# Kernel tuning notes

Hardware: AMD Instinct MI355X
Metric: run time of the kernel (lower is better)

The kernel has to match this reference:

```python
import jax, jax.numpy as jnp
import numpy as np

D_MODEL = 1024
NUM_HEADS = 16
D_K = D_MODEL // NUM_HEADS
BATCH = 2
SEQ = 2048


def setup_inputs() -> dict:
    key = jax.random.key(0)
    ks = jax.random.split(key, 11)
    s = 1.0 / np.sqrt(D_MODEL)
    return {
        "query": jax.random.normal(ks[0], (BATCH, SEQ, D_MODEL), jnp.float32),
        "key_": jax.random.normal(ks[1], (BATCH, SEQ, D_MODEL), jnp.float32),
        "value": jax.random.normal(ks[2], (BATCH, SEQ, D_MODEL), jnp.float32),
        "w_q": jax.random.uniform(ks[3], (D_MODEL, D_MODEL), jnp.float32, -s, s),
        "b_q": jax.random.uniform(ks[4], (D_MODEL,), jnp.float32, -s, s),
        "w_k": jax.random.uniform(ks[5], (D_MODEL, D_MODEL), jnp.float32, -s, s),
        "b_k": jax.random.uniform(ks[6], (D_MODEL,), jnp.float32, -s, s),
        "w_v": jax.random.uniform(ks[7], (D_MODEL, D_MODEL), jnp.float32, -s, s),
        "b_v": jax.random.uniform(ks[8], (D_MODEL,), jnp.float32, -s, s),
        "w_o": jax.random.uniform(ks[9], (D_MODEL, D_MODEL), jnp.float32, -s, s),
        "b_o": jax.random.uniform(ks[10], (D_MODEL,), jnp.float32, -s, s),
    }


def reference(query, key_, value, w_q, b_q, w_k, b_k, w_v, b_v, w_o, b_o):
    B, S, D = query.shape
    H, dk = NUM_HEADS, D_K

    def proj(x, w, b):
        # torch Linear: x @ w.T + b ; reshape to (B, H, S, dk)
        return (x @ w.T + b).reshape(B, S, H, dk).transpose(0, 2, 1, 3)

    Q = proj(query, w_q, b_q)
    K = proj(key_, w_k, b_k)
    V = proj(value, w_v, b_v)

    scores = jnp.einsum("bhqd,bhkd->bhqk", Q, K) / jnp.sqrt(jnp.float32(dk))
    attn = jax.nn.softmax(scores, axis=-1)  # dropout is identity in eval
    ctx = jnp.einsum("bhqk,bhkd->bhqd", attn, V)
    ctx = ctx.transpose(0, 2, 1, 3).reshape(B, S, D)
    out = ctx @ w_o.T + b_o
    return out
```

## Files before the change

kernel.cpp:

```cpp
#include <hip/hip_runtime.h>
#include <cstdint>
#include <cstddef>

typedef unsigned short u16;
typedef short bf16x8 __attribute__((ext_vector_type(8)));
typedef unsigned short u16x8 __attribute__((ext_vector_type(8)));
typedef float f32x4 __attribute__((ext_vector_type(4)));

#define NHEAD 16
#define SEQ 2048
#define DMODEL 1024
#define BATCH 2
#define QSCALE 0.18033688011112042f

__device__ __forceinline__ float exp2_fast(float x) {
  return __builtin_amdgcn_exp2f(x);
}

__device__ __forceinline__ u16 f2bf(float f) {
  union { float f; unsigned u; } v; v.f = f;
  return (u16)((v.u + 0x7fffu + ((v.u >> 16) & 1u)) >> 16);
}

__device__ __forceinline__ unsigned cvt_pk(float a, float b) {
  unsigned r;
  asm("v_cvt_pk_bf16_f32 %0, %1, %2" : "=v"(r) : "v"(a), "v"(b));
  return r;
}

__device__ __forceinline__ int swz(int row, int colbyte) {
  return (row << 7) + (colbyte ^ ((row & 7) << 4));
}

__device__ __forceinline__ void load_lds16(const void* g, void* lds) {
  __builtin_amdgcn_global_load_lds(
      (const __attribute__((address_space(1))) unsigned int*)g,
      (__attribute__((address_space(3))) unsigned int*)lds, 16, 0, 0);
}

__global__ __launch_bounds__(256) void wconv(
    const float* __restrict__ wq, const float* __restrict__ wk,
    const float* __restrict__ wv, const float* __restrict__ wo,
    u16* __restrict__ Wq, u16* __restrict__ Wk, u16* __restrict__ Wv,
    u16* __restrict__ Wo) {
  int bid = blockIdx.x;
  int a = bid >> 9;
  int local = bid & 511;
  const float* in = a == 0 ? wq : a == 1 ? wk : a == 2 ? wv : wo;
  u16* out = a == 0 ? Wq : a == 1 ? Wk : a == 2 ? Wv : Wo;
  int i = local * 256 + threadIdx.x;
  const float4* p = (const float4*)in + (size_t)i * 2;
  float4 a4 = p[0], b4 = p[1];
  u16x8 o;
  o[0] = f2bf(a4.x); o[1] = f2bf(a4.y); o[2] = f2bf(a4.z); o[3] = f2bf(a4.w);
  o[4] = f2bf(b4.x); o[5] = f2bf(b4.y); o[6] = f2bf(b4.z); o[7] = f2bf(b4.w);
  *((u16x8*)out + i) = o;
}

__global__ __launch_bounds__(256) void gemm_qkv(
    const float* __restrict__ A0, const float* __restrict__ A1, const float* __restrict__ A2,
    const u16* __restrict__ W0, const u16* __restrict__ W1, const u16* __restrict__ W2,
    const float* __restrict__ b0, const float* __restrict__ b1, const float* __restrict__ b2,
    u16* __restrict__ C0, u16* __restrict__ C1, u16* __restrict__ C2) {
  constexpr int K = 1024;
  __shared__ u16 Ash[128 * 32];
  __shared__ u16 Bsh[128 * 32];
  const int z = blockIdx.z;
  const float* A = z == 0 ? A0 : z == 1 ? A1 : A2;
  const u16* W = z == 0 ? W0 : z == 1 ? W1 : W2;
  const float* bias = z == 0 ? b0 : z == 1 ? b1 : b2;
  u16* C = z == 0 ? C0 : z == 1 ? C1 : C2;
  const float scale = z == 0 ? QSCALE : 1.0f;

  const int t = threadIdx.x;
  const int w = t >> 6;
  const int l = t & 63;
  const int m0 = (blockIdx.x * 4 + (blockIdx.y >> 3)) * 128;
  const int n0 = (blockIdx.y & 7) * 128;
  const int wm = (w >> 1) * 64;
  const int wn = (w & 1) * 64;
  const int lr = l & 15;
  const int hi = l >> 4;
  const int lk = hi * 8;
  const int srow = l >> 2;
  const int scol = (l & 3) * 8;
  const int ssw = ((l >> 3) & 3) << 3;
  const int ar = t >> 2;
  const int ac = (t & 3) * 8;
  const int asw = ((ar >> 1) & 3) << 3;
  const int fsw = ((lr >> 1) & 3) << 3;

  f32x4 acc[4][4] = {};

  const float* Abase0 = A + (size_t)(m0 + ar) * K;
  const float* Abase1 = A + (size_t)(m0 + 64 + ar) * K;
  f32x4 f0 = *(const f32x4*)&Abase0[ac];
  f32x4 f1 = *(const f32x4*)&Abase0[ac + 4];
  f32x4 f2 = *(const f32x4*)&Abase1[ac];
  f32x4 f3 = *(const f32x4*)&Abase1[ac + 4];

  for (int k0 = 0; k0 < K; k0 += 32) {
#pragma unroll
    for (int c = 0; c < 2; ++c) {
      int rb = (c * 4 + w) * 16 + srow;
      load_lds16(W + (size_t)(n0 + rb) * K + k0 + (scol ^ ssw), &Bsh[(c * 4 + w) * 512]);
    }
    {
      uint4 o;
      o.x = cvt_pk(f0[0], f0[1]); o.y = cvt_pk(f0[2], f0[3]);
      o.z = cvt_pk(f1[0], f1[1]); o.w = cvt_pk(f1[2], f1[3]);
      *(uint4*)&Ash[ar * 32 + (ac ^ asw)] = o;
      o.x = cvt_pk(f2[0], f2[1]); o.y = cvt_pk(f2[2], f2[3]);
      o.z = cvt_pk(f3[0], f3[1]); o.w = cvt_pk(f3[2], f3[3]);
      *(uint4*)&Ash[(64 + ar) * 32 + (ac ^ asw)] = o;
    }
    if (k0 + 32 < K) {
      f0 = *(const f32x4*)&Abase0[k0 + 32 + ac];
      f1 = *(const f32x4*)&Abase0[k0 + 32 + ac + 4];
      f2 = *(const f32x4*)&Abase1[k0 + 32 + ac];
      f3 = *(const f32x4*)&Abase1[k0 + 32 + ac + 4];
    }
    __syncthreads();
    bf16x8 af[4], bfr[4];
#pragma unroll
    for (int i = 0; i < 4; ++i)
      af[i] = *(const bf16x8*)&Ash[(wm + i * 16 + lr) * 32 + (lk ^ fsw)];
#pragma unroll
    for (int j = 0; j < 4; ++j)
      bfr[j] = *(const bf16x8*)&Bsh[(wn + j * 16 + lr) * 32 + (lk ^ fsw)];
#pragma unroll
    for (int i = 0; i < 4; ++i)
#pragma unroll
      for (int j = 0; j < 4; ++j)
        acc[i][j] = __builtin_amdgcn_mfma_f32_16x16x32_bf16(af[i], bfr[j], acc[i][j], 0, 0, 0);
    __syncthreads();
  }

#pragma unroll
  for (int i = 0; i < 4; ++i)
#pragma unroll
    for (int j = 0; j < 4; ++j)
#pragma unroll
      for (int r = 0; r < 4; ++r) {
        int row = m0 + wm + i * 16 + hi * 4 + r;
        int col = n0 + wn + j * 16 + lr;
        float v = (acc[i][j][r] + bias[col]) * scale;
        int b = row >> 11, s = row & 2047;
        int h = col >> 6, d = col & 63;
        C[(((size_t)(b * NHEAD + h) * SEQ + s) << 6) + d] = f2bf(v);
      }
}

__global__ __launch_bounds__(256) void gemm_o(const u16* __restrict__ A,
                                              const u16* __restrict__ W,
                                              const float* __restrict__ bias,
                                              float* __restrict__ C) {
  constexpr int K = 1024;
  __shared__ u16 Ash[64 * 32];
  __shared__ u16 Bsh[128 * 32];
  const int t = threadIdx.x;
  const int w = t >> 6;
  const int l = t & 63;
  const int m0 = (blockIdx.x * 8 + (blockIdx.y >> 3)) * 64;
  const int n0 = (blockIdx.y & 7) * 128;
  const int wm = (w >> 1) * 32;
  const int wn = (w & 1) * 64;
  const int lr = l & 15;
  const int hi = l >> 4;
  const int lk = hi * 8;
  const int srow = l >> 2;
  const int scol = (l & 3) * 8;
  const int ssw = ((l >> 3) & 3) << 3;
  const int fsw = ((lr >> 1) & 3) << 3;

  f32x4 acc[2][4] = {};

  for (int k0 = 0; k0 < K; k0 += 32) {
    {
      int ra = w * 16 + srow;
      load_lds16(A + (size_t)(m0 + ra) * K + k0 + (scol ^ ssw), &Ash[w * 512]);
    }
#pragma unroll
    for (int c = 0; c < 2; ++c) {
      int rb = (c * 4 + w) * 16 + srow;
      load_lds16(W + (size_t)(n0 + rb) * K + k0 + (scol ^ ssw), &Bsh[(c * 4 + w) * 512]);
    }
    __syncthreads();
    bf16x8 af[2], bfr[4];
#pragma unroll
    for (int i = 0; i < 2; ++i)
      af[i] = *(const bf16x8*)&Ash[(wm + i * 16 + lr) * 32 + (lk ^ fsw)];
#pragma unroll
    for (int j = 0; j < 4; ++j)
      bfr[j] = *(const bf16x8*)&Bsh[(wn + j * 16 + lr) * 32 + (lk ^ fsw)];
#pragma unroll
    for (int i = 0; i < 2; ++i)
#pragma unroll
      for (int j = 0; j < 4; ++j)
        acc[i][j] = __builtin_amdgcn_mfma_f32_16x16x32_bf16(af[i], bfr[j], acc[i][j], 0, 0, 0);
    __syncthreads();
  }

#pragma unroll
  for (int i = 0; i < 2; ++i)
#pragma unroll
    for (int j = 0; j < 4; ++j)
#pragma unroll
      for (int r = 0; r < 4; ++r) {
        int row = m0 + wm + i * 16 + hi * 4 + r;
        int col = n0 + wn + j * 16 + lr;
        C[(size_t)row * DMODEL + col] = acc[i][j][r] + bias[col];
      }
}

__global__ __launch_bounds__(256) void transpose_v(const u16* __restrict__ V,
                                                   u16* __restrict__ Vt) {
  __shared__ u16 tile[64][72];
  int st = blockIdx.x, bh = blockIdx.y;
  int t = threadIdx.x;
  {
    int s = t >> 2, part = (t & 3) * 16;
    const u16* g = V + (((size_t)bh * SEQ + st * 64 + s) << 6) + part;
    u16x8 v0 = *(const u16x8*)&g[0];
    u16x8 v1 = *(const u16x8*)&g[8];
    *(u16x8*)&tile[s][part] = v0;
    *(u16x8*)&tile[s][part + 8] = v1;
  }
  __syncthreads();
  {
    int d = t >> 2, sp = (t & 3) * 16;
    u16x8 o0, o1;
#pragma unroll
    for (int j = 0; j < 8; ++j) {
      int c0 = sp + j, c1 = sp + 8 + j;
      o0[j] = tile[(c0 & 3) * 16 + (c0 >> 2)][d];
      o1[j] = tile[(c1 & 3) * 16 + (c1 >> 2)][d];
    }
    u16* out = Vt + ((size_t)bh * 64 + d) * SEQ + st * 64 + sp;
    *(u16x8*)&out[0] = o0;
    *(u16x8*)&out[8] = o1;
  }
}

__device__ __forceinline__ void attn_tile(
    int kt, bool pf, const u16* Kg, const u16* Vg, int srow, int scb,
    char* QsB, char* KsC, char* VsC, char* KsN, char* VsN,
    bf16x8 (&qf)[2][2], f32x4 (&acc)[2][4], float (&lsum)[2][4],
    int w, int lr, int hi) {
  u16x8 nk0, nk1, nv0, nv1;
  if (pf) {
    const u16* kg = Kg + (kt + 1) * 4096;
    const u16* vg = Vg + (kt + 1) * 64;
    nk0 = *(const u16x8*)&kg[srow * 64 + scb / 2];
    nk1 = *(const u16x8*)&kg[srow * 64 + scb / 2 + 8];
    nv0 = *(const u16x8*)&vg[(size_t)srow * SEQ + scb / 2];
    nv1 = *(const u16x8*)&vg[(size_t)srow * SEQ + scb / 2 + 8];
  }

  f32x4 sc[2][4] = {};
  __builtin_amdgcn_s_setprio(1);
#pragma unroll
  for (int ks = 0; ks < 2; ++ks) {
    bf16x8 kb[4];
#pragma unroll
    for (int nt = 0; nt < 4; ++nt)
      kb[nt] = *(const bf16x8*)(KsC + swz(nt * 16 + lr, ks * 64 + hi * 16));
#pragma unroll
    for (int mt = 0; mt < 2; ++mt)
#pragma unroll
      for (int nt = 0; nt < 4; ++nt)
        sc[mt][nt] = __builtin_amdgcn_mfma_f32_16x16x32_bf16(qf[mt][ks], kb[nt], sc[mt][nt], 0, 0, 0);
  }
  __builtin_amdgcn_s_setprio(0);

#pragma unroll
  for (int mt = 0; mt < 2; ++mt)
#pragma unroll
    for (int r = 0; r < 4; ++r) {
      int prow = w * 32 + mt * 16 + hi * 4 + r;
      float p0 = exp2_fast(sc[mt][0][r]);
      float p1 = exp2_fast(sc[mt][1][r]);
      float p2 = exp2_fast(sc[mt][2][r]);
      float p3 = exp2_fast(sc[mt][3][r]);
      lsum[mt][r] += (p0 + p1) + (p2 + p3);
      uint2 pk;
      pk.x = cvt_pk(p0, p1);
      pk.y = cvt_pk(p2, p3);
      *(uint2*)(QsB + swz(prow, lr * 8)) = pk;
    }

  asm volatile("" ::: "memory");

  __builtin_amdgcn_s_setprio(1);
#pragma unroll
  for (int ks = 0; ks < 2; ++ks) {
    bf16x8 pa[2], vb[4];
#pragma unroll
    for (int mt = 0; mt < 2; ++mt)
      pa[mt] = *(const bf16x8*)(QsB + swz(w * 32 + mt * 16 + lr, ks * 64 + hi * 16));
#pragma unroll
    for (int nt = 0; nt < 4; ++nt)
      vb[nt] = *(const bf16x8*)(VsC + swz(nt * 16 + lr, ks * 64 + hi * 16));
#pragma unroll
    for (int mt = 0; mt < 2; ++mt)
#pragma unroll
      for (int nt = 0; nt < 4; ++nt)
        acc[mt][nt] = __builtin_amdgcn_mfma_f32_16x16x32_bf16(pa[mt], vb[nt], acc[mt][nt], 0, 0, 0);
  }
  __builtin_amdgcn_s_setprio(0);

  if (pf) {
    *(u16x8*)(KsN + swz(srow, scb)) = nk0;
    *(u16x8*)(KsN + swz(srow, scb + 16)) = nk1;
    *(u16x8*)(VsN + swz(srow, scb)) = nv0;
    *(u16x8*)(VsN + swz(srow, scb + 16)) = nv1;
  }
  __syncthreads();
}

__global__ __launch_bounds__(256) void attn(const u16* __restrict__ Q,
                                            const u16* __restrict__ K,
                                            const u16* __restrict__ Vt,
                                            u16* __restrict__ ctx) {
  __shared__ u16 Qs[128 * 64];
  __shared__ u16 Ks[2][64 * 64];
  __shared__ u16 Vs[2][64 * 64];
  char* const QsB = (char*)Qs;

  const int t = threadIdx.x, w = t >> 6, l = t & 63;
  const int lr = l & 15, hi = l >> 4;

  const int bid = blockIdx.x;
  const int idx = bid >> 3;
  const int bh = (bid & 7) * 4 + (idx >> 4);
  const int q0 = (idx & 15) * 128;

  const u16* Qg = Q + ((size_t)bh * SEQ + q0) * 64;
  const u16* Kg = K + (size_t)bh * SEQ * 64;
  const u16* Vg = Vt + (size_t)bh * 64 * SEQ;

#pragma unroll
  for (int i = 0; i < 4; ++i) {
    int c = i * 256 + t;
    int row = c >> 3, cb = (c & 7) * 16;
    u16x8 qv = *(const u16x8*)&Qg[row * 64 + cb / 2];
    *(u16x8*)(QsB + swz(row, cb)) = qv;
  }
  const int srow = t >> 2;
  const int scb = (t & 3) * 32;
  {
    u16x8 k0 = *(const u16x8*)&Kg[srow * 64 + scb / 2];
    u16x8 k1 = *(const u16x8*)&Kg[srow * 64 + scb / 2 + 8];
    u16x8 v0 = *(const u16x8*)&Vg[(size_t)srow * SEQ + scb / 2];
    u16x8 v1 = *(const u16x8*)&Vg[(size_t)srow * SEQ + scb / 2 + 8];
    char* KsB = (char*)Ks[0];
    char* VsB = (char*)Vs[0];
    *(u16x8*)(KsB + swz(srow, scb)) = k0;
    *(u16x8*)(KsB + swz(srow, scb + 16)) = k1;
    *(u16x8*)(VsB + swz(srow, scb)) = v0;
    *(u16x8*)(VsB + swz(srow, scb + 16)) = v1;
  }
  __syncthreads();

  bf16x8 qf[2][2];
#pragma unroll
  for (int mt = 0; mt < 2; ++mt)
#pragma unroll
    for (int ks = 0; ks < 2; ++ks)
      qf[mt][ks] = *(const bf16x8*)(QsB + swz(w * 32 + mt * 16 + lr, ks * 64 + hi * 16));

  f32x4 acc[2][4] = {};
  float lsum[2][4] = {{0.f, 0.f, 0.f, 0.f}, {0.f, 0.f, 0.f, 0.f}};

  for (int kt2 = 0; kt2 < SEQ / 128; ++kt2) {
    attn_tile(2 * kt2, true, Kg, Vg, srow, scb, QsB,
              (char*)Ks[0], (char*)Vs[0], (char*)Ks[1], (char*)Vs[1],
              qf, acc, lsum, w, lr, hi);
    attn_tile(2 * kt2 + 1, kt2 < SEQ / 128 - 1, Kg, Vg, srow, scb, QsB,
              (char*)Ks[1], (char*)Vs[1], (char*)Ks[0], (char*)Vs[0],
              qf, acc, lsum, w, lr, hi);
  }

  const int b = bh >> 4, h = bh & 15;
#pragma unroll
  for (int mt = 0; mt < 2; ++mt)
#pragma unroll
    for (int r = 0; r < 4; ++r) {
      float s = lsum[mt][r];
      s += __shfl_xor(s, 1);
      s += __shfl_xor(s, 2);
      s += __shfl_xor(s, 4);
      s += __shfl_xor(s, 8);
      float inv = 1.0f / s;
      int srow_ = q0 + w * 32 + mt * 16 + hi * 4 + r;
#pragma unroll
      for (int nt = 0; nt < 4; ++nt) {
        int d = nt * 16 + lr;
        ctx[((size_t)(b * SEQ + srow_)) * DMODEL + h * 64 + d] =
            f2bf(acc[mt][nt][r] * inv);
      }
    }
}

extern "C" void kernel_launch(void* const* d_in, const int* in_sizes, int n_in,
                              void* d_out, int out_size, void* d_ws, size_t ws_size,
                              hipStream_t stream) {
  const float* q  = (const float*)d_in[0];
  const float* k  = (const float*)d_in[1];
  const float* v  = (const float*)d_in[2];
  const float* wq = (const float*)d_in[3];
  const float* bq = (const float*)d_in[4];
  const float* wk = (const float*)d_in[5];
  const float* bk = (const float*)d_in[6];
  const float* wv = (const float*)d_in[7];
  const float* bv = (const float*)d_in[8];
  const float* wo = (const float*)d_in[9];
  const float* bo = (const float*)d_in[10];

  const size_t XB = (size_t)4096 * 1024 * 2;
  const size_t WB = (size_t)1024 * 1024 * 2;
  char* ws = (char*)d_ws;
  u16* ctxb = (u16*)(ws);
  u16* Vtb = (u16*)(ws + XB);
  u16* Wq = (u16*)(ws + 3 * XB);
  u16* Wk = (u16*)(ws + 3 * XB + WB);
  u16* Wv = (u16*)(ws + 3 * XB + 2 * WB);
  u16* Wo = (u16*)(ws + 3 * XB + 3 * WB);
  u16* Qb = (u16*)(ws + 4 * XB);
  u16* Kb = (u16*)(ws + 5 * XB);
  u16* Vb = (u16*)(ws + 6 * XB);

  wconv<<<2048, 256, 0, stream>>>(wq, wk, wv, wo, Wq, Wk, Wv, Wo);

  gemm_qkv<<<dim3(8, 32, 3), 256, 0, stream>>>(q, k, v, Wq, Wk, Wv,
                                               bq, bk, bv, Qb, Kb, Vb);

  transpose_v<<<dim3(SEQ / 64, BATCH * NHEAD), 256, 0, stream>>>(Vb, Vtb);

  attn<<<512, 256, 0, stream>>>(Qb, Kb, Vtb, ctxb);

  gemm_o<<<dim3(8, 64), 256, 0, stream>>>(ctxb, Wo, bo, (float*)d_out);
}
```

Measured before the change: 117.5 us.

## Split attention over two KV halves and merge partials in a combine kernel

Each attention block now processes only half of the key/value sequence, so the grid grows from 512 to 1024 blocks. Each block writes an unnormalised partial context in bf16 plus its per-row exp-sum. A new combine kernel adds the two partials and divides by the total sum before the output projection. This is meant to raise parallelism and occupancy in the attention stage, at the cost of an extra kernel launch, extra global traffic for the partial buffers, and an extra bf16 rounding of the unnormalised partials.

```diff
diff --git a/kernel.cpp b/kernel.cpp
--- a/kernel.cpp
+++ b/kernel.cpp
@@ -20,6 +20,10 @@
 __device__ __forceinline__ u16 f2bf(float f) {
   union { float f; unsigned u; } v; v.f = f;
   return (u16)((v.u + 0x7fffu + ((v.u >> 16) & 1u)) >> 16);
+}
+
+__device__ __forceinline__ float bf2f(u16 x) {
+  union { unsigned u; float f; } v; v.u = ((unsigned)x) << 16; return v.f;
 }
 
 __device__ __forceinline__ unsigned cvt_pk(float a, float b) {
@@ -321,7 +325,9 @@
 __global__ __launch_bounds__(256) void attn(const u16* __restrict__ Q,
                                             const u16* __restrict__ K,
                                             const u16* __restrict__ Vt,
-                                            u16* __restrict__ ctx) {
+                                            u16* __restrict__ N1,
+                                            u16* __restrict__ N2,
+                                            float* __restrict__ Lb) {
   __shared__ u16 Qs[128 * 64];
   __shared__ u16 Ks[2][64 * 64];
   __shared__ u16 Vs[2][64 * 64];
@@ -332,8 +338,11 @@
 
   const int bid = blockIdx.x;
   const int idx = bid >> 3;
-  const int bh = (bid & 7) * 4 + (idx >> 4);
-  const int q0 = (idx & 15) * 128;
+  const int bh = (bid & 7) * 4 + (idx >> 5);
+  const int rem = idx & 31;
+  const int q0 = (rem >> 1) * 128;
+  const int half = rem & 1;
+  const int base = half * 16;
 
   const u16* Qg = Q + ((size_t)bh * SEQ + q0) * 64;
   const u16* Kg = K + (size_t)bh * SEQ * 64;
@@ -349,10 +358,12 @@
   const int srow = t >> 2;
   const int scb = (t & 3) * 32;
   {
-    u16x8 k0 = *(const u16x8*)&Kg[srow * 64 + scb / 2];
-    u16x8 k1 = *(const u16x8*)&Kg[srow * 64 + scb / 2 + 8];
-    u16x8 v0 = *(const u16x8*)&Vg[(size_t)srow * SEQ + scb / 2];
-    u16x8 v1 = *(const u16x8*)&Vg[(size_t)srow * SEQ + scb / 2 + 8];
+    const u16* kg = Kg + base * 4096;
+    const u16* vg = Vg + base * 64;
+    u16x8 k0 = *(const u16x8*)&kg[srow * 64 + scb / 2];
+    u16x8 k1 = *(const u16x8*)&kg[srow * 64 + scb / 2 + 8];
+    u16x8 v0 = *(const u16x8*)&vg[(size_t)srow * SEQ + scb / 2];
+    u16x8 v1 = *(const u16x8*)&vg[(size_t)srow * SEQ + scb / 2 + 8];
     char* KsB = (char*)Ks[0];
     char* VsB = (char*)Vs[0];
     *(u16x8*)(KsB + swz(srow, scb)) = k0;
@@ -372,16 +383,17 @@
   f32x4 acc[2][4] = {};
   float lsum[2][4] = {{0.f, 0.f, 0.f, 0.f}, {0.f, 0.f, 0.f, 0.f}};
 
-  for (int kt2 = 0; kt2 < SEQ / 128; ++kt2) {
-    attn_tile(2 * kt2, true, Kg, Vg, srow, scb, QsB,
+  for (int kt2 = 0; kt2 < 8; ++kt2) {
+    attn_tile(base + 2 * kt2, true, Kg, Vg, srow, scb, QsB,
               (char*)Ks[0], (char*)Vs[0], (char*)Ks[1], (char*)Vs[1],
               qf, acc, lsum, w, lr, hi);
-    attn_tile(2 * kt2 + 1, kt2 < SEQ / 128 - 1, Kg, Vg, srow, scb, QsB,
+    attn_tile(base + 2 * kt2 + 1, kt2 < 7, Kg, Vg, srow, scb, QsB,
               (char*)Ks[1], (char*)Vs[1], (char*)Ks[0], (char*)Vs[0],
               qf, acc, lsum, w, lr, hi);
   }
 
   const int b = bh >> 4, h = bh & 15;
+  u16* Np = half ? N2 : N1;
 #pragma unroll
   for (int mt = 0; mt < 2; ++mt)
 #pragma unroll
@@ -391,15 +403,35 @@
       s += __shfl_xor(s, 2);
       s += __shfl_xor(s, 4);
       s += __shfl_xor(s, 8);
-      float inv = 1.0f / s;
       int srow_ = q0 + w * 32 + mt * 16 + hi * 4 + r;
+      if (lr == 0) Lb[half * (32 * SEQ) + bh * SEQ + srow_] = s;
 #pragma unroll
       for (int nt = 0; nt < 4; ++nt) {
         int d = nt * 16 + lr;
-        ctx[((size_t)(b * SEQ + srow_)) * DMODEL + h * 64 + d] =
-            f2bf(acc[mt][nt][r] * inv);
+        Np[((size_t)(b * SEQ + srow_)) * DMODEL + h * 64 + d] =
+            f2bf(acc[mt][nt][r]);
       }
     }
+}
+
+__global__ __launch_bounds__(256) void combine(u16* N1,
+                                               const u16* __restrict__ N2,
+                                               const float* __restrict__ Lb) {
+  int i8 = blockIdx.x * 256 + threadIdx.x;
+  int row = i8 >> 7;
+  int col8 = i8 & 127;
+  int h = col8 >> 3;
+  int b = row >> 11, s = row & 2047;
+  int bh = b * NHEAD + h;
+  float lsum = Lb[bh * SEQ + s] + Lb[32 * SEQ + bh * SEQ + s];
+  float inv = 1.0f / lsum;
+  u16x8 n1 = *((const u16x8*)N1 + i8);
+  u16x8 n2 = *((const u16x8*)N2 + i8);
+  u16x8 o;
+#pragma unroll
+  for (int j = 0; j < 8; ++j)
+    o[j] = f2bf((bf2f(n1[j]) + bf2f(n2[j])) * inv);
+  *((u16x8*)N1 + i8) = o;
 }
 
 extern "C" void kernel_launch(void* const* d_in, const int* in_sizes, int n_in,
@@ -420,8 +452,9 @@
   const size_t XB = (size_t)4096 * 1024 * 2;
   const size_t WB = (size_t)1024 * 1024 * 2;
   char* ws = (char*)d_ws;
-  u16* ctxb = (u16*)(ws);
+  u16* N1b = (u16*)(ws);
   u16* Vtb = (u16*)(ws + XB);
+  u16* N2b = (u16*)(ws + 2 * XB);
   u16* Wq = (u16*)(ws + 3 * XB);
   u16* Wk = (u16*)(ws + 3 * XB + WB);
   u16* Wv = (u16*)(ws + 3 * XB + 2 * WB);
@@ -429,6 +462,7 @@
   u16* Qb = (u16*)(ws + 4 * XB);
   u16* Kb = (u16*)(ws + 5 * XB);
   u16* Vb = (u16*)(ws + 6 * XB);
+  float* Lbuf = (float*)(ws + 6 * XB);
 
   wconv<<<2048, 256, 0, stream>>>(wq, wk, wv, wo, Wq, Wk, Wv, Wo);
 
@@ -437,7 +471,9 @@
 
   transpose_v<<<dim3(SEQ / 64, BATCH * NHEAD), 256, 0, stream>>>(Vb, Vtb);
 
-  attn<<<512, 256, 0, stream>>>(Qb, Kb, Vtb, ctxb);
-
-  gemm_o<<<dim3(8, 64), 256, 0, stream>>>(ctxb, Wo, bo, (float*)d_out);
-}
+  attn<<<1024, 256, 0, stream>>>(Qb, Kb, Vtb, N1b, N2b, Lbuf);
+
+  combine<<<2048, 256, 0, stream>>>(N1b, N2b, Lbuf);
+
+  gemm_o<<<dim3(8, 64), 256, 0, stream>>>(N1b, Wo, bo, (float*)d_out);
+}
```

Measured after the change: 125.2 us. 1.07x slower.
